# Kernel optimization log

Measured on AMD Instinct MI355X. Metric: run time of the kernel, lower is better.

## Reference

```python
import jax, jax.numpy as jnp
import numpy as np

N_HEADS = 16
N_KV_HEADS = 8
N_REP = 2
HEAD_DIM = 128
SOFTCAP = 50.0
NEG_INF = -2.3819763e38
ROPE_BASE = 10000.0


def _rotate_half(x):
    x1, x2 = jnp.split(x, 2, axis=-1)
    return jnp.concatenate((-x2, x1), axis=-1)


def _rope_cos_sin(seq_len, dtype):
    # Gemma2RotaryEmbedding: inv_freq over even dims, emb = cat(freqs, freqs)
    inv_freq = 1.0 / (ROPE_BASE ** (jnp.arange(0, HEAD_DIM, 2, dtype=jnp.float32) / HEAD_DIM))
    freqs = jnp.arange(seq_len, dtype=jnp.float32)[:, None] * inv_freq[None, :]  # [s, hd/2]
    emb = jnp.concatenate((freqs, freqs), axis=-1)  # [s, hd]
    return jnp.cos(emb).astype(dtype), jnp.sin(emb).astype(dtype)


def setup_inputs() -> dict:
    key = jax.random.key(0)
    ks = jax.random.split(key, 5)
    b, s, d = 2, 2048, 2048
    w_scale = 0.02
    return {
        "x": jax.random.normal(ks[0], (b, s, d), dtype=jnp.float32),
        "wq": jax.random.normal(ks[1], (N_HEADS * HEAD_DIM, d), dtype=jnp.float32) * w_scale,
        "wk": jax.random.normal(ks[2], (N_KV_HEADS * HEAD_DIM, d), dtype=jnp.float32) * w_scale,
        "wv": jax.random.normal(ks[3], (N_KV_HEADS * HEAD_DIM, d), dtype=jnp.float32) * w_scale,
        "wo": jax.random.normal(ks[4], (d, N_HEADS * HEAD_DIM), dtype=jnp.float32) * w_scale,
    }


def reference(x, wq, wk, wv, wo):
    b, s, d = x.shape
    # QKV projections (linear_fn = plain x @ W.T)
    xq = (x @ wq.T).reshape(b, s, N_HEADS, HEAD_DIM).transpose(0, 2, 1, 3)      # [b,h,s,hd]
    xk = (x @ wk.T).reshape(b, s, N_KV_HEADS, HEAD_DIM).transpose(0, 2, 1, 3)   # [b,kv,s,hd]
    xv = (x @ wv.T).reshape(b, s, N_KV_HEADS, HEAD_DIM).transpose(0, 2, 1, 3)
    # Gemma2 rotary on q, k
    cos, sin = _rope_cos_sin(s, x.dtype)  # [s,hd] each, broadcast over b,h
    xq = xq * cos + _rotate_half(xq) * sin
    xk = xk * cos + _rotate_half(xk) * sin
    # repeat_kv: expand kv heads to n_heads
    keys = jnp.repeat(xk, N_REP, axis=1)
    values = jnp.repeat(xv, N_REP, axis=1)
    # scores with scaling and Gemma2 logit softcapping
    scale = float(HEAD_DIM) ** -0.5
    scores = jnp.einsum("bhsd,bhtd->bhst", xq * scale, keys)
    scores = jnp.tanh(scores / SOFTCAP) * SOFTCAP
    # causal additive mask [s, t]
    q_pos = jnp.arange(s)[:, None]
    k_pos = jnp.arange(s)[None, :]
    mask = jnp.where(k_pos <= q_pos, 0.0, NEG_INF).astype(jnp.float32)
    scores = scores + mask  # broadcast over [b,h]
    probs = jax.nn.softmax(scores.astype(jnp.float32), axis=-1).astype(xq.dtype)
    out = jnp.einsum("bhst,bhtd->bhsd", probs, values)
    out = out.transpose(0, 2, 1, 3).reshape(b, s, N_HEADS * HEAD_DIM)
    return out @ wo.T
```

## Files before the change

kernel.cpp:

```cpp
#include <hip/hip_runtime.h>
#include <stdint.h>
#include <stddef.h>

#define S_LEN   2048
#define DMODEL  2048
#define NHEADS  16
#define NKVH    8
#define HD      128
#define QPRE 1.7677669529663688e-3f
#define C1 72.13475204444817f

typedef __attribute__((ext_vector_type(8))) short  short8;
typedef __attribute__((ext_vector_type(4))) float  float4v;

static __device__ __forceinline__ unsigned short f2bf(float f) {
  union { float f; unsigned int u; } v; v.f = f;
  unsigned int u = v.u;
  u += 0x7fffu + ((u >> 16) & 1u);
  return (unsigned short)(u >> 16);
}
static __device__ __forceinline__ float bf2f(unsigned short b) {
  union { unsigned int u; float f; } v; v.u = ((unsigned int)b) << 16;
  return v.f;
}
static __device__ __forceinline__ void gload_lds16(const void* g, void* l) {
  __builtin_amdgcn_global_load_lds(
      (const __attribute__((address_space(1))) void*)g,
      (__attribute__((address_space(3))) void*)l, 16, 0, 0);
}

__global__ __launch_bounds__(256) void cvt_all(
    const float* __restrict__ x,  const float* __restrict__ wq,
    const float* __restrict__ wk, const float* __restrict__ wv,
    const float* __restrict__ wo,
    ushort4* __restrict__ xb, ushort4* __restrict__ wcat,
    ushort4* __restrict__ wob) {
  int i = blockIdx.x * 256 + threadIdx.x;
  const float4* src; ushort4* dst; int j;
  if (i < 2097152)      { src = (const float4*)x;  dst = xb;             j = i; }
  else if (i < 3145728) { src = (const float4*)wq; dst = wcat;           j = i - 2097152; }
  else if (i < 3670016) { src = (const float4*)wk; dst = wcat + 1048576; j = i - 3145728; }
  else if (i < 4194304) { src = (const float4*)wv; dst = wcat + 1572864; j = i - 3670016; }
  else                  { src = (const float4*)wo; dst = wob;            j = i - 4194304; }
  float4 v = src[j];
  ushort4 o;
  o.x = f2bf(v.x); o.y = f2bf(v.y); o.z = f2bf(v.z); o.w = f2bf(v.w);
  dst[j] = o;
}

__global__ __launch_bounds__(256, 2) void gemm_bf16(
    const unsigned short* __restrict__ A,
    const unsigned short* __restrict__ B,
    void* __restrict__ Cout, int N, int mode) {
  const int t    = threadIdx.x;
  const int lane = t & 63;
  const int w    = t >> 6;
  const int l15  = lane & 15;
  const int quad = lane >> 4;
  const int m0   = blockIdx.y * 128;
  const int n0   = blockIdx.x * 128;
  const int wm   = (w >> 1) * 64;
  const int wn   = (w & 1) * 64;

  __shared__ unsigned short At[128 * 32];
  __shared__ unsigned short Bt[128 * 32];

  float4v acc[4][4];
#pragma unroll
  for (int mt = 0; mt < 4; ++mt)
#pragma unroll
    for (int nt = 0; nt < 4; ++nt)
      acc[mt][nt] = (float4v){0.f, 0.f, 0.f, 0.f};

  const unsigned short* Abase = A + (size_t)m0 * DMODEL;
  const unsigned short* Bbase = B + (size_t)n0 * DMODEL;
  const int srow = w * 16 + (lane >> 2);
  const int sch  = (lane & 3) * 8;

  for (int k0 = 0; k0 < DMODEL; k0 += 32) {
#pragma unroll
    for (int r = 0; r < 2; ++r) {
      gload_lds16(Abase + (size_t)(r * 64 + srow) * DMODEL + k0 + sch,
                  At + (r * 256 + w * 64) * 8);
      gload_lds16(Bbase + (size_t)(r * 64 + srow) * DMODEL + k0 + sch,
                  Bt + (r * 256 + w * 64) * 8);
    }
    __syncthreads();
    short8 af[4], bf[4];
#pragma unroll
    for (int mt = 0; mt < 4; ++mt)
      af[mt] = *(const short8*)(At + (wm + mt * 16 + l15) * 32 + quad * 8);
#pragma unroll
    for (int nt = 0; nt < 4; ++nt)
      bf[nt] = *(const short8*)(Bt + (wn + nt * 16 + l15) * 32 + quad * 8);
#pragma unroll
    for (int mt = 0; mt < 4; ++mt)
#pragma unroll
      for (int nt = 0; nt < 4; ++nt)
        acc[mt][nt] = __builtin_amdgcn_mfma_f32_16x16x32_bf16(
            af[mt], bf[nt], acc[mt][nt], 0, 0, 0);
    __syncthreads();
  }

  if (mode == 2) {
    float* C = (float*)Cout;
#pragma unroll
    for (int mt = 0; mt < 4; ++mt) {
      int row = m0 + wm + mt * 16 + quad * 4;
#pragma unroll
      for (int nt = 0; nt < 4; ++nt) {
        int col = n0 + wn + nt * 16 + l15;
#pragma unroll
        for (int r2 = 0; r2 < 4; ++r2)
          C[(size_t)(row + r2) * N + col] = acc[mt][nt][r2];
      }
    }
  } else {
    unsigned short* C = (unsigned short*)Cout;
#pragma unroll
    for (int mt = 0; mt < 4; ++mt) {
      int row0 = m0 + wm + mt * 16 + quad * 4;
      int b = row0 >> 11, s0 = row0 & (S_LEN - 1);
#pragma unroll
      for (int nt = 0; nt < 4; ++nt) {
        int col = n0 + wn + nt * 16 + l15;
        if (col < 2048) {
          int head = col >> 7, d = col & (HD - 1);
#pragma unroll
          for (int r2 = 0; r2 < 4; ++r2)
            C[((size_t)(b * 16 + head) * S_LEN + s0 + r2) * HD + d] =
                f2bf(acc[mt][nt][r2]);
        } else if (col < 3072) {
          int c2 = col - 2048;
          int kvh = c2 >> 7, d = c2 & (HD - 1);
#pragma unroll
          for (int r2 = 0; r2 < 4; ++r2)
            C[8388608 + ((size_t)(b * 8 + kvh) * S_LEN + s0 + r2) * HD + d] =
                f2bf(acc[mt][nt][r2]);
        } else {
          int c2 = col - 3072;
          int kvh = c2 >> 7, d = c2 & (HD - 1);
          ushort4 pk;
          pk.x = f2bf(acc[mt][nt][0]); pk.y = f2bf(acc[mt][nt][1]);
          pk.z = f2bf(acc[mt][nt][2]); pk.w = f2bf(acc[mt][nt][3]);
          *(ushort4*)&C[12582912 + ((size_t)(b * 8 + kvh) * HD + d) * S_LEN + s0] = pk;
        }
      }
    }
  }
}

__global__ __launch_bounds__(256) void rope_kernel(unsigned short* __restrict__ Q,
                                                   unsigned short* __restrict__ Kc) {
  int gt = blockIdx.x * 256 + threadIdx.x;
  int r = gt >> 6;
  int j = gt & 63;
  const int QROWS = 2 * NHEADS * S_LEN;
  bool isQ = (r < QROWS);
  unsigned short* p = isQ ? (Q + (size_t)r * HD)
                          : (Kc + (size_t)(r - QROWS) * HD);
  int pos = r & (S_LEN - 1);
  float inv = exp2f(-(float)j * 0.20762050593046868f);
  float ang = (float)pos * inv;
  float c = cosf(ang), s = sinf(ang);
  float sc = isQ ? QPRE : 1.0f;
  float x1 = bf2f(p[j]), x2 = bf2f(p[j + 64]);
  p[j]      = f2bf((x1 * c - x2 * s) * sc);
  p[j + 64] = f2bf((x2 * c + x1 * s) * sc);
}

__global__ __launch_bounds__(128) void attn_kernel(
    const unsigned short* __restrict__ Q,
    const unsigned short* __restrict__ Kc,
    const unsigned short* __restrict__ Vt,
    unsigned short* __restrict__ Aout) {
  const int t    = threadIdx.x;
  const int lane = t & 63;
  const int w    = t >> 6;
  const int l15  = lane & 15;
  const int quad = lane >> 4;
  const int bh = blockIdx.x;
  const int pp = blockIdx.y;
  const int b = bh >> 4, h = bh & 15, kv = h >> 1;
  const int qtA = pp, qtB = 31 - pp;
  const int q0A = qtA * 64, q0B = qtB * 64;
  const int ntB = qtB + 1;

  __shared__ unsigned short Kt[64 * 128];
  __shared__ unsigned short Vts[128 * 64];
  __shared__ unsigned short Pt[2 * 2 * 2048];

  int offK[8], offV[8];
#pragma unroll
  for (int i = 0; i < 8; ++i) {
    int g = i * 128 + t;
    int rK = g >> 4, cK = (g & 15) ^ (rK & 7);
    offK[i] = rK * HD + cK * 8;
    int rV = g >> 3, cV = (g & 7) ^ (rV & 7);
    offV[i] = rV * S_LEN + cV * 8;
  }

  const unsigned short* QA = Q + ((size_t)(b * NHEADS + h) * S_LEN + q0A + w * 32) * HD;
  const unsigned short* QB = Q + ((size_t)(b * NHEADS + h) * S_LEN + q0B + w * 32) * HD;
  short8 qfA[2][4], qfB[2][4];
#pragma unroll
  for (int ntq = 0; ntq < 2; ++ntq)
#pragma unroll
    for (int kk = 0; kk < 4; ++kk) {
      qfA[ntq][kk] = *(const short8*)&QA[(ntq * 16 + l15) * HD + kk * 32 + quad * 8];
      qfB[ntq][kk] = *(const short8*)&QB[(ntq * 16 + l15) * HD + kk * 32 + quad * 8];
    }

  float4v oA[2][8], oB[2][8];
#pragma unroll
  for (int ntq = 0; ntq < 2; ++ntq)
#pragma unroll
    for (int nth = 0; nth < 8; ++nth) {
      oA[ntq][nth] = (float4v){0.f, 0.f, 0.f, 0.f};
      oB[ntq][nth] = (float4v){0.f, 0.f, 0.f, 0.f};
    }
  float lsA[2] = {0.f, 0.f}, lsB[2] = {0.f, 0.f};

  const unsigned short* kg0 = Kc + (size_t)(b * NKVH + kv) * S_LEN * HD;
  const unsigned short* vg0 = Vt + (size_t)(b * NKVH + kv) * HD * S_LEN;
  unsigned short* PB = Pt + (w * 2 + 0) * 2048;
  unsigned short* PA = Pt + (w * 2 + 1) * 2048;

  auto stage = [&](int kt) {
    const unsigned short* kgp = kg0 + (size_t)kt * 64 * HD;
    const unsigned short* vgp = vg0 + (size_t)kt * 64;
#pragma unroll
    for (int i = 0; i < 8; ++i)
      gload_lds16(kgp + offK[i], &Kt[(i * 128 + w * 64) * 8]);
#pragma unroll
    for (int i = 0; i < 8; ++i)
      gload_lds16(vgp + offV[i], &Vts[(i * 128 + w * 64) * 8]);
  };

  auto softcap = [&](float x) -> float {
    float xx = __builtin_amdgcn_fmed3f(x, -0.26f, 0.26f);
    float x2 = xx * xx;
    float u = __builtin_fmaf(0.13333334f, x2, -0.33333334f);
    float v = __builtin_fmaf(u, x2, 1.0f);
    return __builtin_amdgcn_exp2f((C1 * xx) * v);
  };

  stage(0);
  for (int kt = 0; kt < ntB; ++kt) {
    __syncthreads();
    const bool doA   = (kt <= qtA);
    const bool diagA = (kt == qtA);
    const bool diagB = (kt == qtB);

#pragma unroll
    for (int ntk = 0; ntk < 4; ++ntk) {
      int pb = l15 * 64 + (((ntk * 2 + (quad >> 1)) ^ (l15 & 7)) * 8) + (quad & 1) * 4;
      short8 kf[4];
#pragma unroll
      for (int kk = 0; kk < 4; ++kk)
        kf[kk] = *(const short8*)
            &Kt[(ntk * 16 + l15) * HD + (((kk * 4 + quad) ^ (l15 & 7)) * 8)];

      if (diagB && (ntk * 16 > w * 32 + 31)) {
        uint2 z; z.x = 0u; z.y = 0u;
        *(uint2*)&PB[pb] = z; *(uint2*)&PB[pb + 1024] = z;
      } else {
        float4v s0 = (float4v){0.f, 0.f, 0.f, 0.f}, s1 = s0;
#pragma unroll
        for (int kk = 0; kk < 4; ++kk) {
          s0 = __builtin_amdgcn_mfma_f32_16x16x32_bf16(kf[kk], qfB[0][kk], s0, 0, 0, 0);
          s1 = __builtin_amdgcn_mfma_f32_16x16x32_bf16(kf[kk], qfB[1][kk], s1, 0, 0, 0);
        }
#pragma unroll
        for (int ntq = 0; ntq < 2; ++ntq) {
          const float4v& sv = ntq ? s1 : s0;
          float pv[4];
#pragma unroll
          for (int r = 0; r < 4; ++r) {
            float p = softcap(sv[r]);
            if (diagB)
              p = (ntk * 16 + quad * 4 + r <= w * 32 + ntq * 16 + l15) ? p : 0.f;
            lsB[ntq] += p;
            pv[r] = p;
          }
          union { float f; unsigned u; } u0, u1, u2, u3;
          u0.f = pv[0]; u1.f = pv[1]; u2.f = pv[2]; u3.f = pv[3];
          uint2 pk;
          pk.x = __builtin_amdgcn_perm(u1.u, u0.u, 0x07060302);
          pk.y = __builtin_amdgcn_perm(u3.u, u2.u, 0x07060302);
          *(uint2*)&PB[pb + ntq * 1024] = pk;
        }
      }

      if (doA) {
        if (diagA && (ntk * 16 > w * 32 + 31)) {
          uint2 z; z.x = 0u; z.y = 0u;
          *(uint2*)&PA[pb] = z; *(uint2*)&PA[pb + 1024] = z;
        } else {
          float4v s0 = (float4v){0.f, 0.f, 0.f, 0.f}, s1 = s0;
#pragma unroll
          for (int kk = 0; kk < 4; ++kk) {
            s0 = __builtin_amdgcn_mfma_f32_16x16x32_bf16(kf[kk], qfA[0][kk], s0, 0, 0, 0);
            s1 = __builtin_amdgcn_mfma_f32_16x16x32_bf16(kf[kk], qfA[1][kk], s1, 0, 0, 0);
          }
#pragma unroll
          for (int ntq = 0; ntq < 2; ++ntq) {
            const float4v& sv = ntq ? s1 : s0;
            float pv[4];
#pragma unroll
            for (int r = 0; r < 4; ++r) {
              float p = softcap(sv[r]);
              if (diagA)
                p = (ntk * 16 + quad * 4 + r <= w * 32 + ntq * 16 + l15) ? p : 0.f;
              lsA[ntq] += p;
              pv[r] = p;
            }
            union { float f; unsigned u; } u0, u1, u2, u3;
            u0.f = pv[0]; u1.f = pv[1]; u2.f = pv[2]; u3.f = pv[3];
            uint2 pk;
            pk.x = __builtin_amdgcn_perm(u1.u, u0.u, 0x07060302);
            pk.y = __builtin_amdgcn_perm(u3.u, u2.u, 0x07060302);
            *(uint2*)&PA[pb + ntq * 1024] = pk;
          }
        }
      }
    }

#pragma unroll
    for (int kk = 0; kk < 2; ++kk) {
      int sw = ((kk * 4 + quad) ^ (l15 & 7)) * 8;
      short8 pB0 = *(const short8*)&PB[l15 * 64 + sw];
      short8 pB1 = *(const short8*)&PB[(16 + l15) * 64 + sw];
      short8 pA0, pA1;
      if (doA) {
        pA0 = *(const short8*)&PA[l15 * 64 + sw];
        pA1 = *(const short8*)&PA[(16 + l15) * 64 + sw];
      }
#pragma unroll
      for (int nth = 0; nth < 8; ++nth) {
        short8 vf = *(const short8*)&Vts[(nth * 16 + l15) * 64 + sw];
        oB[0][nth] = __builtin_amdgcn_mfma_f32_16x16x32_bf16(pB0, vf, oB[0][nth], 0, 0, 0);
        oB[1][nth] = __builtin_amdgcn_mfma_f32_16x16x32_bf16(pB1, vf, oB[1][nth], 0, 0, 0);
        if (doA) {
          oA[0][nth] = __builtin_amdgcn_mfma_f32_16x16x32_bf16(pA0, vf, oA[0][nth], 0, 0, 0);
          oA[1][nth] = __builtin_amdgcn_mfma_f32_16x16x32_bf16(pA1, vf, oA[1][nth], 0, 0, 0);
        }
      }
    }
    __syncthreads();
    if (kt + 1 < ntB) stage(kt + 1);
  }

#pragma unroll
  for (int tile = 0; tile < 2; ++tile) {
    float (&ls)[2] = tile ? lsA : lsB;
    float4v (&oo)[2][8] = tile ? oA : oB;
    int q0 = tile ? q0A : q0B;
    float inv[2];
#pragma unroll
    for (int ntq = 0; ntq < 2; ++ntq) {
      float v = ls[ntq];
      v += __shfl_xor(v, 16, 64);
      v += __shfl_xor(v, 32, 64);
      inv[ntq] = __builtin_amdgcn_rcpf(v);
    }
    unsigned short* ob = Aout + (size_t)(b * S_LEN + q0 + w * 32) * DMODEL + h * HD;
#pragma unroll
    for (int ntq = 0; ntq < 2; ++ntq) {
      float iv[4];
#pragma unroll
      for (int r = 0; r < 4; ++r) iv[r] = __shfl(inv[ntq], quad * 4 + r, 64);
#pragma unroll
      for (int nth = 0; nth < 8; ++nth) {
#pragma unroll
        for (int r = 0; r < 4; ++r) {
          int row = ntq * 16 + quad * 4 + r;
          ob[(size_t)row * DMODEL + nth * 16 + l15] = f2bf(oo[ntq][nth][r] * iv[r]);
        }
      }
    }
  }
}

extern "C" void kernel_launch(void* const* d_in, const int* in_sizes, int n_in,
                              void* d_out, int out_size, void* d_ws, size_t ws_size,
                              hipStream_t stream) {
  const float* x  = (const float*)d_in[0];
  const float* wq = (const float*)d_in[1];
  const float* wk = (const float*)d_in[2];
  const float* wv = (const float*)d_in[3];
  const float* wo = (const float*)d_in[4];

  char* ws = (char*)d_ws;
  unsigned short* xb   = (unsigned short*)(ws + 0);
  unsigned short* wcat = (unsigned short*)(ws + 16777216);
  unsigned short* wob  = (unsigned short*)(ws + 33554432);
  unsigned short* QKV  = (unsigned short*)(ws + 41943040);
  unsigned short* AO   = (unsigned short*)(ws + 75497472);

  unsigned short* Qw = QKV;
  unsigned short* Kw = QKV + 8388608;
  unsigned short* Vw = QKV + 12582912;

  cvt_all<<<20480, 256, 0, stream>>>(x, wq, wk, wv, wo,
                                     (ushort4*)xb, (ushort4*)wcat, (ushort4*)wob);

  gemm_bf16<<<dim3(32, 32), 256, 0, stream>>>(xb, wcat, QKV, 4096, 3);

  rope_kernel<<<24576, 256, 0, stream>>>(Qw, Kw);

  attn_kernel<<<dim3(32, 16), 128, 0, stream>>>(Qw, Kw, Vw, AO);

  gemm_bf16<<<dim3(16, 32), 256, 0, stream>>>(AO, wob, d_out, 2048, 2);
}
```

Before: 345.3 us.

## Double-buffer K/V tiles and split attention block across four waves

The attention kernel now runs four waves per block, each owning 16 query rows instead of 32, which halves the accumulator registers per wave and allows two blocks per CU. K and V tiles are double-buffered in LDS and the next tile is prefetched right after the barrier, so loads overlap with compute and one barrier per iteration is removed. The cost is twice the K/V LDS footprint, and each K fragment read from LDS is now reused across fewer query rows.

Measured after the change: 338.1 us. 2.1% less time.

```diff
diff --git a/kernel.cpp b/kernel.cpp
--- a/kernel.cpp
+++ b/kernel.cpp
@@ -169,7 +169,7 @@
   p[j + 64] = f2bf((x2 * c + x1 * s) * sc);
 }
 
-__global__ __launch_bounds__(128) void attn_kernel(
+__global__ __launch_bounds__(256, 2) void attn_kernel(
     const unsigned short* __restrict__ Q,
     const unsigned short* __restrict__ Kc,
     const unsigned short* __restrict__ Vt,
@@ -186,55 +186,51 @@
   const int q0A = qtA * 64, q0B = qtB * 64;
   const int ntB = qtB + 1;
 
-  __shared__ unsigned short Kt[64 * 128];
-  __shared__ unsigned short Vts[128 * 64];
-  __shared__ unsigned short Pt[2 * 2 * 2048];
-
-  int offK[8], offV[8];
-#pragma unroll
-  for (int i = 0; i < 8; ++i) {
-    int g = i * 128 + t;
+  __shared__ unsigned short Kt[2][64 * 128];
+  __shared__ unsigned short Vts[2][128 * 64];
+  __shared__ unsigned short Pt[4 * 2 * 1024];
+
+  int offK[4], offV[4];
+#pragma unroll
+  for (int i = 0; i < 4; ++i) {
+    int g = i * 256 + t;
     int rK = g >> 4, cK = (g & 15) ^ (rK & 7);
     offK[i] = rK * HD + cK * 8;
     int rV = g >> 3, cV = (g & 7) ^ (rV & 7);
     offV[i] = rV * S_LEN + cV * 8;
   }
 
-  const unsigned short* QA = Q + ((size_t)(b * NHEADS + h) * S_LEN + q0A + w * 32) * HD;
-  const unsigned short* QB = Q + ((size_t)(b * NHEADS + h) * S_LEN + q0B + w * 32) * HD;
-  short8 qfA[2][4], qfB[2][4];
-#pragma unroll
-  for (int ntq = 0; ntq < 2; ++ntq)
-#pragma unroll
-    for (int kk = 0; kk < 4; ++kk) {
-      qfA[ntq][kk] = *(const short8*)&QA[(ntq * 16 + l15) * HD + kk * 32 + quad * 8];
-      qfB[ntq][kk] = *(const short8*)&QB[(ntq * 16 + l15) * HD + kk * 32 + quad * 8];
-    }
-
-  float4v oA[2][8], oB[2][8];
-#pragma unroll
-  for (int ntq = 0; ntq < 2; ++ntq)
-#pragma unroll
-    for (int nth = 0; nth < 8; ++nth) {
-      oA[ntq][nth] = (float4v){0.f, 0.f, 0.f, 0.f};
-      oB[ntq][nth] = (float4v){0.f, 0.f, 0.f, 0.f};
-    }
-  float lsA[2] = {0.f, 0.f}, lsB[2] = {0.f, 0.f};
+  const unsigned short* QA = Q + ((size_t)(b * NHEADS + h) * S_LEN + q0A + w * 16) * HD;
+  const unsigned short* QB = Q + ((size_t)(b * NHEADS + h) * S_LEN + q0B + w * 16) * HD;
+  short8 qfA[4], qfB[4];
+#pragma unroll
+  for (int kk = 0; kk < 4; ++kk) {
+    qfA[kk] = *(const short8*)&QA[l15 * HD + kk * 32 + quad * 8];
+    qfB[kk] = *(const short8*)&QB[l15 * HD + kk * 32 + quad * 8];
+  }
+
+  float4v oA[8], oB[8];
+#pragma unroll
+  for (int nth = 0; nth < 8; ++nth) {
+    oA[nth] = (float4v){0.f, 0.f, 0.f, 0.f};
+    oB[nth] = (float4v){0.f, 0.f, 0.f, 0.f};
+  }
+  float lsA = 0.f, lsB = 0.f;
 
   const unsigned short* kg0 = Kc + (size_t)(b * NKVH + kv) * S_LEN * HD;
   const unsigned short* vg0 = Vt + (size_t)(b * NKVH + kv) * HD * S_LEN;
-  unsigned short* PB = Pt + (w * 2 + 0) * 2048;
-  unsigned short* PA = Pt + (w * 2 + 1) * 2048;
-
-  auto stage = [&](int kt) {
+  unsigned short* PB = Pt + (w * 2 + 0) * 1024;
+  unsigned short* PA = Pt + (w * 2 + 1) * 1024;
+
+  auto stage = [&](int kt, int buf) {
     const unsigned short* kgp = kg0 + (size_t)kt * 64 * HD;
     const unsigned short* vgp = vg0 + (size_t)kt * 64;
 #pragma unroll
-    for (int i = 0; i < 8; ++i)
-      gload_lds16(kgp + offK[i], &Kt[(i * 128 + w * 64) * 8]);
-#pragma unroll
-    for (int i = 0; i < 8; ++i)
-      gload_lds16(vgp + offV[i], &Vts[(i * 128 + w * 64) * 8]);
+    for (int i = 0; i < 4; ++i)
+      gload_lds16(kgp + offK[i], &Kt[buf][(i * 256 + w * 64) * 8]);
+#pragma unroll
+    for (int i = 0; i < 4; ++i)
+      gload_lds16(vgp + offV[i], &Vts[buf][(i * 256 + w * 64) * 8]);
   };
 
   auto softcap = [&](float x) -> float {
@@ -245,12 +241,16 @@
     return __builtin_amdgcn_exp2f((C1 * xx) * v);
   };
 
-  stage(0);
+  stage(0, 0);
   for (int kt = 0; kt < ntB; ++kt) {
+    const int cur = kt & 1;
     __syncthreads();
+    if (kt + 1 < ntB) stage(kt + 1, cur ^ 1);
     const bool doA   = (kt <= qtA);
     const bool diagA = (kt == qtA);
     const bool diagB = (kt == qtB);
+    const unsigned short* Kb = Kt[cur];
+    const unsigned short* Vb = Vts[cur];
 
 #pragma unroll
     for (int ntk = 0; ntk < 4; ++ntk) {
@@ -259,28 +259,49 @@
 #pragma unroll
       for (int kk = 0; kk < 4; ++kk)
         kf[kk] = *(const short8*)
-            &Kt[(ntk * 16 + l15) * HD + (((kk * 4 + quad) ^ (l15 & 7)) * 8)];
-
-      if (diagB && (ntk * 16 > w * 32 + 31)) {
+            &Kb[(ntk * 16 + l15) * HD + (((kk * 4 + quad) ^ (l15 & 7)) * 8)];
+
+      if (diagB && (ntk * 16 > w * 16 + 15)) {
         uint2 z; z.x = 0u; z.y = 0u;
-        *(uint2*)&PB[pb] = z; *(uint2*)&PB[pb + 1024] = z;
+        *(uint2*)&PB[pb] = z;
       } else {
-        float4v s0 = (float4v){0.f, 0.f, 0.f, 0.f}, s1 = s0;
-#pragma unroll
-        for (int kk = 0; kk < 4; ++kk) {
-          s0 = __builtin_amdgcn_mfma_f32_16x16x32_bf16(kf[kk], qfB[0][kk], s0, 0, 0, 0);
-          s1 = __builtin_amdgcn_mfma_f32_16x16x32_bf16(kf[kk], qfB[1][kk], s1, 0, 0, 0);
+        float4v s0 = (float4v){0.f, 0.f, 0.f, 0.f};
+#pragma unroll
+        for (int kk = 0; kk < 4; ++kk)
+          s0 = __builtin_amdgcn_mfma_f32_16x16x32_bf16(kf[kk], qfB[kk], s0, 0, 0, 0);
+        float pv[4];
+#pragma unroll
+        for (int r = 0; r < 4; ++r) {
+          float p = softcap(s0[r]);
+          if (diagB)
+            p = (ntk * 16 + quad * 4 + r <= w * 16 + l15) ? p : 0.f;
+          lsB += p;
+          pv[r] = p;
         }
-#pragma unroll
-        for (int ntq = 0; ntq < 2; ++ntq) {
-          const float4v& sv = ntq ? s1 : s0;
+        union { float f; unsigned u; } u0, u1, u2, u3;
+        u0.f = pv[0]; u1.f = pv[1]; u2.f = pv[2]; u3.f = pv[3];
+        uint2 pk;
+        pk.x = __builtin_amdgcn_perm(u1.u, u0.u, 0x07060302);
+        pk.y = __builtin_amdgcn_perm(u3.u, u2.u, 0x07060302);
+        *(uint2*)&PB[pb] = pk;
+      }
+
+      if (doA) {
+        if (diagA && (ntk * 16 > w * 16 + 15)) {
+          uint2 z; z.x = 0u; z.y = 0u;
+          *(uint2*)&PA[pb] = z;
+        } else {
+          float4v s0 = (float4v){0.f, 0.f, 0.f, 0.f};
+#pragma unroll
+          for (int kk = 0; kk < 4; ++kk)
+            s0 = __builtin_amdgcn_mfma_f32_16x16x32_bf16(kf[kk], qfA[kk], s0, 0, 0, 0);
           float pv[4];
 #pragma unroll
           for (int r = 0; r < 4; ++r) {
-            float p = softcap(sv[r]);
-            if (diagB)
-              p = (ntk * 16 + quad * 4 + r <= w * 32 + ntq * 16 + l15) ? p : 0.f;
-            lsB[ntq] += p;
+            float p = softcap(s0[r]);
+            if (diagA)
+              p = (ntk * 16 + quad * 4 + r <= w * 16 + l15) ? p : 0.f;
+            lsA += p;
             pv[r] = p;
           }
           union { float f; unsigned u; } u0, u1, u2, u3;
@@ -288,40 +309,7 @@
           uint2 pk;
           pk.x = __builtin_amdgcn_perm(u1.u, u0.u, 0x07060302);
           pk.y = __builtin_amdgcn_perm(u3.u, u2.u, 0x07060302);
-          *(uint2*)&PB[pb + ntq * 1024] = pk;
-        }
-      }
-
-      if (doA) {
-        if (diagA && (ntk * 16 > w * 32 + 31)) {
-          uint2 z; z.x = 0u; z.y = 0u;
-          *(uint2*)&PA[pb] = z; *(uint2*)&PA[pb + 1024] = z;
-        } else {
-          float4v s0 = (float4v){0.f, 0.f, 0.f, 0.f}, s1 = s0;
-#pragma unroll
-          for (int kk = 0; kk < 4; ++kk) {
-            s0 = __builtin_amdgcn_mfma_f32_16x16x32_bf16(kf[kk], qfA[0][kk], s0, 0, 0, 0);
-            s1 = __builtin_amdgcn_mfma_f32_16x16x32_bf16(kf[kk], qfA[1][kk], s1, 0, 0, 0);
-          }
-#pragma unroll
-          for (int ntq = 0; ntq < 2; ++ntq) {
-            const float4v& sv = ntq ? s1 : s0;
-            float pv[4];
-#pragma unroll
-            for (int r = 0; r < 4; ++r) {
-              float p = softcap(sv[r]);
-              if (diagA)
-                p = (ntk * 16 + quad * 4 + r <= w * 32 + ntq * 16 + l15) ? p : 0.f;
-              lsA[ntq] += p;
-              pv[r] = p;
-            }
-            union { float f; unsigned u; } u0, u1, u2, u3;
-            u0.f = pv[0]; u1.f = pv[1]; u2.f = pv[2]; u3.f = pv[3];
-            uint2 pk;
-            pk.x = __builtin_amdgcn_perm(u1.u, u0.u, 0x07060302);
-            pk.y = __builtin_amdgcn_perm(u3.u, u2.u, 0x07060302);
-            *(uint2*)&PA[pb + ntq * 1024] = pk;
-          }
+          *(uint2*)&PA[pb] = pk;
         }
       }
     }
@@ -330,53 +318,37 @@
     for (int kk = 0; kk < 2; ++kk) {
       int sw = ((kk * 4 + quad) ^ (l15 & 7)) * 8;
       short8 pB0 = *(const short8*)&PB[l15 * 64 + sw];
-      short8 pB1 = *(const short8*)&PB[(16 + l15) * 64 + sw];
-      short8 pA0, pA1;
-      if (doA) {
-        pA0 = *(const short8*)&PA[l15 * 64 + sw];
-        pA1 = *(const short8*)&PA[(16 + l15) * 64 + sw];
-      }
+      short8 pA0;
+      if (doA) pA0 = *(const short8*)&PA[l15 * 64 + sw];
 #pragma unroll
       for (int nth = 0; nth < 8; ++nth) {
-        short8 vf = *(const short8*)&Vts[(nth * 16 + l15) * 64 + sw];
-        oB[0][nth] = __builtin_amdgcn_mfma_f32_16x16x32_bf16(pB0, vf, oB[0][nth], 0, 0, 0);
-        oB[1][nth] = __builtin_amdgcn_mfma_f32_16x16x32_bf16(pB1, vf, oB[1][nth], 0, 0, 0);
-        if (doA) {
-          oA[0][nth] = __builtin_amdgcn_mfma_f32_16x16x32_bf16(pA0, vf, oA[0][nth], 0, 0, 0);
-          oA[1][nth] = __builtin_amdgcn_mfma_f32_16x16x32_bf16(pA1, vf, oA[1][nth], 0, 0, 0);
-        }
-      }
-    }
-    __syncthreads();
-    if (kt + 1 < ntB) stage(kt + 1);
+        short8 vf = *(const short8*)&Vb[(nth * 16 + l15) * 64 + sw];
+        oB[nth] = __builtin_amdgcn_mfma_f32_16x16x32_bf16(pB0, vf, oB[nth], 0, 0, 0);
+        if (doA)
+          oA[nth] = __builtin_amdgcn_mfma_f32_16x16x32_bf16(pA0, vf, oA[nth], 0, 0, 0);
+      }
+    }
   }
 
 #pragma unroll
   for (int tile = 0; tile < 2; ++tile) {
-    float (&ls)[2] = tile ? lsA : lsB;
-    float4v (&oo)[2][8] = tile ? oA : oB;
+    float ls = tile ? lsA : lsB;
+    float4v* oo = tile ? oA : oB;
     int q0 = tile ? q0A : q0B;
-    float inv[2];
-#pragma unroll
-    for (int ntq = 0; ntq < 2; ++ntq) {
-      float v = ls[ntq];
-      v += __shfl_xor(v, 16, 64);
-      v += __shfl_xor(v, 32, 64);
-      inv[ntq] = __builtin_amdgcn_rcpf(v);
-    }
-    unsigned short* ob = Aout + (size_t)(b * S_LEN + q0 + w * 32) * DMODEL + h * HD;
-#pragma unroll
-    for (int ntq = 0; ntq < 2; ++ntq) {
-      float iv[4];
-#pragma unroll
-      for (int r = 0; r < 4; ++r) iv[r] = __shfl(inv[ntq], quad * 4 + r, 64);
-#pragma unroll
-      for (int nth = 0; nth < 8; ++nth) {
-#pragma unroll
-        for (int r = 0; r < 4; ++r) {
-          int row = ntq * 16 + quad * 4 + r;
-          ob[(size_t)row * DMODEL + nth * 16 + l15] = f2bf(oo[ntq][nth][r] * iv[r]);
-        }
+    float v = ls;
+    v += __shfl_xor(v, 16, 64);
+    v += __shfl_xor(v, 32, 64);
+    float inv = __builtin_amdgcn_rcpf(v);
+    float iv[4];
+#pragma unroll
+    for (int r = 0; r < 4; ++r) iv[r] = __shfl(inv, quad * 4 + r, 64);
+    unsigned short* ob = Aout + (size_t)(b * S_LEN + q0 + w * 16) * DMODEL + h * HD;
+#pragma unroll
+    for (int nth = 0; nth < 8; ++nth) {
+#pragma unroll
+      for (int r = 0; r < 4; ++r) {
+        int row = quad * 4 + r;
+        ob[(size_t)row * DMODEL + nth * 16 + l15] = f2bf(oo[nth][r] * iv[r]);
       }
     }
   }
@@ -409,7 +381,7 @@
 
   rope_kernel<<<24576, 256, 0, stream>>>(Qw, Kw);
 
-  attn_kernel<<<dim3(32, 16), 128, 0, stream>>>(Qw, Kw, Vw, AO);
+  attn_kernel<<<dim3(32, 16), 256, 0, stream>>>(Qw, Kw, Vw, AO);
 
   gemm_bf16<<<dim3(16, 32), 256, 0, stream>>>(AO, wob, d_out, 2048, 2);
 }
```
